# Performance work log

Hardware: AMD Instinct MI355X
Metric: run time of the kernel (lower is better)

The kernel has to match this reference:

```python
import jax, jax.numpy as jnp
import numpy as np

OUT_FEATURES = 8192
PACKED_IN = 4096          # in_features = 2 * PACKED_IN = 8192
GROUP_SIZE = 128
N_GROUPS = (2 * PACKED_IN) // GROUP_SIZE  # 64


def _unpack_int4(packed):
    """Unpack bytes (stored as int32 in [0,256)) into signed int4 pairs [O, 2P].

    Matches torch: high nibble first, then low nibble, both sign-corrected
    (values >= 8 map to value - 16).
    """
    high = packed >> 4
    low = packed & 15
    high = jnp.where(high >= 8, high - 16, high)
    low = jnp.where(low >= 8, low - 16, low)
    return jnp.stack([high, low], axis=-1).reshape(packed.shape[0], -1)


def setup_inputs() -> dict:
    key = jax.random.key(0)
    k1, k2, k3, k4, k5 = jax.random.split(key, 5)
    x = jax.random.normal(k1, (1, 128, 2 * PACKED_IN), dtype=jnp.float32)
    weight_q = jax.random.randint(k2, (OUT_FEATURES, PACKED_IN), 0, 256, dtype=jnp.int32)
    # small positive per-group scales, float zero points (as in the torch module)
    scale = jax.random.uniform(k3, (OUT_FEATURES, N_GROUPS), dtype=jnp.float32) * 0.05 + 1e-3
    zero_point = jax.random.normal(k4, (OUT_FEATURES, N_GROUPS), dtype=jnp.float32)
    bias = jax.random.normal(k5, (OUT_FEATURES,), dtype=jnp.float32)
    return {"x": x, "weight_q": weight_q, "scale": scale, "zero_point": zero_point, "bias": bias}


def reference(x, weight_q, scale, zero_point, bias):
    O = weight_q.shape[0]
    w = _unpack_int4(weight_q).astype(jnp.float32)          # [O, in]
    wg = w.reshape(O, N_GROUPS, GROUP_SIZE)                  # group view
    # (w - zp) * scale, broadcast per group (== repeat_interleave in torch)
    W = ((wg - zero_point[:, :, None]) * scale[:, :, None]).reshape(O, -1)
    return jnp.einsum('bsi,oi->bso', x, W) + bias
```

## Files before the change

### kernel.cpp

```cpp
#include <hip/hip_runtime.h>
#include <hip/hip_bf16.h>
#include <stdint.h>

#define M_DIM 128
#define N_DIM 8192
#define K_DIM 8192
#define KP    4096
#define NGRP  64
#define KSPLIT 8
#define KCHUNK (K_DIM / KSPLIT)
#define BK    64
#define NSTEPS (KCHUNK / BK)

typedef __attribute__((ext_vector_type(8))) short bf16x8;
typedef __attribute__((ext_vector_type(4))) float f32x4;

__device__ __forceinline__ unsigned short f2bf(float f) {
  unsigned int u = __float_as_uint(f);
  return (unsigned short)((u + 0x7fffu + ((u >> 16) & 1u)) >> 16);
}

__global__ void xcast_kernel(const float* __restrict__ x, unsigned short* __restrict__ xb) {
  int idx = (blockIdx.x * blockDim.x + threadIdx.x) * 8;
  const float4* xp = (const float4*)(x + idx);
  float4 a = xp[0], b = xp[1];
  uint4 o;
  o.x = (unsigned)f2bf(a.x) | ((unsigned)f2bf(a.y) << 16);
  o.y = (unsigned)f2bf(a.z) | ((unsigned)f2bf(a.w) << 16);
  o.z = (unsigned)f2bf(b.x) | ((unsigned)f2bf(b.y) << 16);
  o.w = (unsigned)f2bf(b.z) | ((unsigned)f2bf(b.w) << 16);
  *(uint4*)(xb + idx) = o;
}

__global__ __launch_bounds__(512, 4)
void gemm_kernel(const unsigned short* __restrict__ xb,
                 const int* __restrict__ wq,
                 const float* __restrict__ scale,
                 const float* __restrict__ zpt,
                 unsigned short* __restrict__ partial)
{
  __shared__ uint4 xtile[2][1024];
  __shared__ uint4 wtile[2][1024];

  const int tid = threadIdx.x;
  const int l   = tid & 63;
  const int w   = tid >> 6;
  const int wm  = w >> 2;
  const int wn  = w & 3;
  const int l15 = l & 15;
  const int lk  = l >> 4;
  const int n0  = blockIdx.x * 128;
  const int ks  = blockIdx.y;
  const int k0  = ks * KCHUNK;

  const int r0 = n0 + wn * 32 + l15;
  const int r1 = r0 + 16;

  const float* sp0 = scale + r0 * NGRP + ks * 8;
  const float* zp0 = zpt   + r0 * NGRP + ks * 8;
  const float* sp1 = scale + r1 * NGRP + ks * 8;
  const float* zp1 = zpt   + r1 * NGRP + ks * 8;
  float4 s0a = *(const float4*)sp0,     s0b = *(const float4*)(sp0 + 4);
  float4 z0a = *(const float4*)zp0,     z0b = *(const float4*)(zp0 + 4);
  float4 s1a = *(const float4*)sp1,     s1b = *(const float4*)(sp1 + 4);
  float4 z1a = *(const float4*)zp1,     z1b = *(const float4*)(zp1 + 4);

  auto STAGE = [&](int t, int nb) {
    const int kt = k0 + t * BK;
    #pragma unroll
    for (int i = 0; i < 2; ++i) {
      int c = i * 512 + tid;
      int row = c >> 3, q = (c & 7) ^ (row & 7);
      const unsigned short* src = xb + (size_t)row * K_DIM + kt + q * 8;
      uint4* dst = &xtile[nb][i * 512 + w * 64];
      __builtin_amdgcn_global_load_lds(
          (__attribute__((address_space(1))) void*)(void*)src,
          (__attribute__((address_space(3))) void*)(void*)dst, 16, 0, 0);
    }
    #pragma unroll
    for (int i = 0; i < 2; ++i) {
      int c = i * 512 + tid;
      int row = c >> 3, q = (c & 7) ^ (row & 7);
      const int* src = wq + (size_t)(n0 + row) * KP + (k0 >> 1) + t * 32 + q * 4;
      uint4* dst = &wtile[nb][i * 512 + w * 64];
      __builtin_amdgcn_global_load_lds(
          (__attribute__((address_space(1))) void*)(void*)src,
          (__attribute__((address_space(3))) void*)(void*)dst, 16, 0, 0);
    }
  };

  f32x4 acc[4][2];
  #pragma unroll
  for (int mi = 0; mi < 4; ++mi)
    #pragma unroll
    for (int ni = 0; ni < 2; ++ni) {
      f32x4 z = {0.f, 0.f, 0.f, 0.f};
      acc[mi][ni] = z;
    }

  STAGE(0, 0);
  STAGE(1, 1);
  float scs0[8] = {s0a.x, s0a.y, s0a.z, s0a.w, s0b.x, s0b.y, s0b.z, s0b.w};
  float scs1[8] = {s1a.x, s1a.y, s1a.z, s1a.w, s1b.x, s1b.y, s1b.z, s1b.w};
  float nzs0[8] = {-z0a.x * s0a.x, -z0a.y * s0a.y, -z0a.z * s0a.z, -z0a.w * s0a.w,
                   -z0b.x * s0b.x, -z0b.y * s0b.y, -z0b.z * s0b.z, -z0b.w * s0b.w};
  float nzs1[8] = {-z1a.x * s1a.x, -z1a.y * s1a.y, -z1a.z * s1a.z, -z1a.w * s1a.w,
                   -z1b.x * s1b.x, -z1b.y * s1b.y, -z1b.z * s1b.z, -z1b.w * s1b.w};

  const int wrow0 = wn * 32 + l15;
  const int wrow1 = wrow0 + 16;

  #pragma unroll
  for (int t = 0; t < NSTEPS; ++t) {
    asm volatile("s_waitcnt vmcnt(4)" ::: "memory");
    __builtin_amdgcn_s_barrier();

    const int cb = t & 1;
    const float sc[2] = {scs0[t >> 1], scs1[t >> 1]};
    const float nz[2] = {nzs0[t >> 1], nzs1[t >> 1]};

    #pragma unroll
    for (int kk = 0; kk < 2; ++kk) {
      const int q = kk * 4 + lk;
      uint4 av[4];
      #pragma unroll
      for (int mi = 0; mi < 4; ++mi) {
        int r = wm * 64 + mi * 16 + l15;
        av[mi] = xtile[cb][r * 8 + (q ^ (r & 7))];
      }
      uint4 pw[2];
      pw[0] = wtile[cb][wrow0 * 8 + (q ^ (wrow0 & 7))];
      pw[1] = wtile[cb][wrow1 * 8 + (q ^ (wrow1 & 7))];
      uint4 bq[2];
      #pragma unroll
      for (int ni = 0; ni < 2; ++ni) {
        int v4[4] = {(int)pw[ni].x, (int)pw[ni].y, (int)pw[ni].z, (int)pw[ni].w};
        unsigned words[4];
        #pragma unroll
        for (int j = 0; j < 4; ++j) {
          int hi = (v4[j] << 24) >> 28;
          int lo = (v4[j] << 28) >> 28;
          float fh = fmaf((float)hi, sc[ni], nz[ni]);
          float fl = fmaf((float)lo, sc[ni], nz[ni]);
          asm("v_cvt_pk_bf16_f32 %0, %1, %2" : "=v"(words[j]) : "v"(fh), "v"(fl));
        }
        uint4 o; o.x = words[0]; o.y = words[1]; o.z = words[2]; o.w = words[3];
        bq[ni] = o;
      }
      #pragma unroll
      for (int mi = 0; mi < 4; ++mi)
        #pragma unroll
        for (int ni = 0; ni < 2; ++ni)
          acc[mi][ni] = __builtin_amdgcn_mfma_f32_16x16x32_bf16(
              __builtin_bit_cast(bf16x8, av[mi]),
              __builtin_bit_cast(bf16x8, bq[ni]),
              acc[mi][ni], 0, 0, 0);
    }

    __builtin_amdgcn_s_barrier();
    STAGE(t + 2 < NSTEPS ? t + 2 : NSTEPS - 1, t & 1);
  }
  asm volatile("s_waitcnt vmcnt(0)" ::: "memory");

  unsigned short* p = partial + (size_t)ks * (M_DIM * N_DIM);
  #pragma unroll
  for (int mi = 0; mi < 4; ++mi)
    #pragma unroll
    for (int ni = 0; ni < 2; ++ni) {
      int col = n0 + wn * 32 + ni * 16 + l15;
      int rowb = wm * 64 + mi * 16 + lk * 4;
      #pragma unroll
      for (int j = 0; j < 4; ++j)
        p[(size_t)(rowb + j) * N_DIM + col] = f2bf(acc[mi][ni][j]);
    }
}

__global__ void reduce_kernel(const unsigned short* __restrict__ part,
                              const float* __restrict__ bias,
                              float* __restrict__ out) {
  int idx = (blockIdx.x * blockDim.x + threadIdx.x) * 8;
  float s[8];
  #pragma unroll
  for (int j = 0; j < 8; ++j) s[j] = 0.f;
  #pragma unroll
  for (int k = 0; k < KSPLIT; ++k) {
    uint4 v = *(const uint4*)(part + (size_t)k * (M_DIM * N_DIM) + idx);
    unsigned ws[4] = {v.x, v.y, v.z, v.w};
    #pragma unroll
    for (int j = 0; j < 4; ++j) {
      s[2 * j]     += __uint_as_float((ws[j] & 0xffffu) << 16);
      s[2 * j + 1] += __uint_as_float(ws[j] & 0xffff0000u);
    }
  }
  int col = idx & (N_DIM - 1);
  float4 b0 = *(const float4*)(bias + col);
  float4 b1 = *(const float4*)(bias + col + 4);
  float4 o0, o1;
  o0.x = s[0] + b0.x; o0.y = s[1] + b0.y; o0.z = s[2] + b0.z; o0.w = s[3] + b0.w;
  o1.x = s[4] + b1.x; o1.y = s[5] + b1.y; o1.z = s[6] + b1.z; o1.w = s[7] + b1.w;
  *(float4*)(out + idx) = o0;
  *(float4*)(out + idx + 4) = o1;
}

extern "C" void kernel_launch(void* const* d_in, const int* in_sizes, int n_in,
                              void* d_out, int out_size, void* d_ws, size_t ws_size,
                              hipStream_t stream) {
  const float* x     = (const float*)d_in[0];
  const int*   wq    = (const int*)d_in[1];
  const float* scale = (const float*)d_in[2];
  const float* zpt   = (const float*)d_in[3];
  const float* bias  = (const float*)d_in[4];
  float* out = (float*)d_out;

  unsigned short* xb = (unsigned short*)d_ws;
  const size_t xbytes = (size_t)M_DIM * K_DIM * 2;
  unsigned short* partial = (unsigned short*)((char*)d_ws + xbytes);

  xcast_kernel<<<(M_DIM * K_DIM) / (256 * 8), 256, 0, stream>>>(x, xb);
  gemm_kernel<<<dim3(N_DIM / 128, KSPLIT), 512, 0, stream>>>(
      xb, wq, scale, zpt, partial);
  reduce_kernel<<<(M_DIM * N_DIM) / (256 * 8), 256, 0, stream>>>(
      partial, bias, out);
}
```

Before: 46.81 us.

## Widen GEMM N tile to 256 to reuse each activation tile across more columns

Doubles the per-block output-column tile from 128 to 256, so each wave computes a 64x64 sub-tile (4x4 MFMA accumulators) instead of 64x32. Each activation tile loaded into LDS is now reused across twice as many weight rows, halving total activation traffic and the grid size. In exchange, register and LDS use per block rise, the launch bound drops to 2 blocks per CU, and the grid shrinks to 256 blocks, which may underfill the GPU's compute units. The wait count is raised to match the extra weight loads per stage.

```diff
diff --git a/kernel.cpp b/kernel.cpp
--- a/kernel.cpp
+++ b/kernel.cpp
@@ -10,6 +10,7 @@
 #define KSPLIT 8
 #define KCHUNK (K_DIM / KSPLIT)
 #define BK    64
+#define BN    256
 #define NSTEPS (KCHUNK / BK)
 
 typedef __attribute__((ext_vector_type(8))) short bf16x8;
@@ -32,7 +33,7 @@
   *(uint4*)(xb + idx) = o;
 }
 
-__global__ __launch_bounds__(512, 4)
+__global__ __launch_bounds__(512, 2)
 void gemm_kernel(const unsigned short* __restrict__ xb,
                  const int* __restrict__ wq,
                  const float* __restrict__ scale,
@@ -40,7 +41,7 @@
                  unsigned short* __restrict__ partial)
 {
   __shared__ uint4 xtile[2][1024];
-  __shared__ uint4 wtile[2][1024];
+  __shared__ uint4 wtile[2][2048];
 
   const int tid = threadIdx.x;
   const int l   = tid & 63;
@@ -49,21 +50,22 @@
   const int wn  = w & 3;
   const int l15 = l & 15;
   const int lk  = l >> 4;
-  const int n0  = blockIdx.x * 128;
+  const int n0  = blockIdx.x * BN;
   const int ks  = blockIdx.y;
   const int k0  = ks * KCHUNK;
 
-  const int r0 = n0 + wn * 32 + l15;
-  const int r1 = r0 + 16;
-
-  const float* sp0 = scale + r0 * NGRP + ks * 8;
-  const float* zp0 = zpt   + r0 * NGRP + ks * 8;
-  const float* sp1 = scale + r1 * NGRP + ks * 8;
-  const float* zp1 = zpt   + r1 * NGRP + ks * 8;
-  float4 s0a = *(const float4*)sp0,     s0b = *(const float4*)(sp0 + 4);
-  float4 z0a = *(const float4*)zp0,     z0b = *(const float4*)(zp0 + 4);
-  float4 s1a = *(const float4*)sp1,     s1b = *(const float4*)(sp1 + 4);
-  float4 z1a = *(const float4*)zp1,     z1b = *(const float4*)(zp1 + 4);
+  int rr[4];
+  #pragma unroll
+  for (int ni = 0; ni < 4; ++ni) rr[ni] = n0 + wn * 64 + ni * 16 + l15;
+
+  float4 sv[4][2], zv[4][2];
+  #pragma unroll
+  for (int ni = 0; ni < 4; ++ni) {
+    const float* sp = scale + rr[ni] * NGRP + ks * 8;
+    const float* zp = zpt   + rr[ni] * NGRP + ks * 8;
+    sv[ni][0] = *(const float4*)sp;  sv[ni][1] = *(const float4*)(sp + 4);
+    zv[ni][0] = *(const float4*)zp;  zv[ni][1] = *(const float4*)(zp + 4);
+  }
 
   auto STAGE = [&](int t, int nb) {
     const int kt = k0 + t * BK;
@@ -78,7 +80,7 @@
           (__attribute__((address_space(3))) void*)(void*)dst, 16, 0, 0);
     }
     #pragma unroll
-    for (int i = 0; i < 2; ++i) {
+    for (int i = 0; i < 4; ++i) {
       int c = i * 512 + tid;
       int row = c >> 3, q = (c & 7) ^ (row & 7);
       const int* src = wq + (size_t)(n0 + row) * KP + (k0 >> 1) + t * 32 + q * 4;
@@ -89,35 +91,36 @@
     }
   };
 
-  f32x4 acc[4][2];
+  f32x4 acc[4][4];
   #pragma unroll
   for (int mi = 0; mi < 4; ++mi)
     #pragma unroll
-    for (int ni = 0; ni < 2; ++ni) {
+    for (int ni = 0; ni < 4; ++ni) {
       f32x4 z = {0.f, 0.f, 0.f, 0.f};
       acc[mi][ni] = z;
     }
 
   STAGE(0, 0);
   STAGE(1, 1);
-  float scs0[8] = {s0a.x, s0a.y, s0a.z, s0a.w, s0b.x, s0b.y, s0b.z, s0b.w};
-  float scs1[8] = {s1a.x, s1a.y, s1a.z, s1a.w, s1b.x, s1b.y, s1b.z, s1b.w};
-  float nzs0[8] = {-z0a.x * s0a.x, -z0a.y * s0a.y, -z0a.z * s0a.z, -z0a.w * s0a.w,
-                   -z0b.x * s0b.x, -z0b.y * s0b.y, -z0b.z * s0b.z, -z0b.w * s0b.w};
-  float nzs1[8] = {-z1a.x * s1a.x, -z1a.y * s1a.y, -z1a.z * s1a.z, -z1a.w * s1a.w,
-                   -z1b.x * s1b.x, -z1b.y * s1b.y, -z1b.z * s1b.z, -z1b.w * s1b.w};
-
-  const int wrow0 = wn * 32 + l15;
-  const int wrow1 = wrow0 + 16;
+  float scs[4][8], nzs[4][8];
+  #pragma unroll
+  for (int ni = 0; ni < 4; ++ni)
+    #pragma unroll
+    for (int h = 0; h < 2; ++h) {
+      float4 s4 = sv[ni][h], z4 = zv[ni][h];
+      scs[ni][h * 4 + 0] = s4.x;  nzs[ni][h * 4 + 0] = -z4.x * s4.x;
+      scs[ni][h * 4 + 1] = s4.y;  nzs[ni][h * 4 + 1] = -z4.y * s4.y;
+      scs[ni][h * 4 + 2] = s4.z;  nzs[ni][h * 4 + 2] = -z4.z * s4.z;
+      scs[ni][h * 4 + 3] = s4.w;  nzs[ni][h * 4 + 3] = -z4.w * s4.w;
+    }
 
   #pragma unroll
   for (int t = 0; t < NSTEPS; ++t) {
-    asm volatile("s_waitcnt vmcnt(4)" ::: "memory");
+    asm volatile("s_waitcnt vmcnt(6)" ::: "memory");
     __builtin_amdgcn_s_barrier();
 
     const int cb = t & 1;
-    const float sc[2] = {scs0[t >> 1], scs1[t >> 1]};
-    const float nz[2] = {nzs0[t >> 1], nzs1[t >> 1]};
+    const int g  = t >> 1;
 
     #pragma unroll
     for (int kk = 0; kk < 2; ++kk) {
@@ -128,20 +131,23 @@
         int r = wm * 64 + mi * 16 + l15;
         av[mi] = xtile[cb][r * 8 + (q ^ (r & 7))];
       }
-      uint4 pw[2];
-      pw[0] = wtile[cb][wrow0 * 8 + (q ^ (wrow0 & 7))];
-      pw[1] = wtile[cb][wrow1 * 8 + (q ^ (wrow1 & 7))];
-      uint4 bq[2];
-      #pragma unroll
-      for (int ni = 0; ni < 2; ++ni) {
+      uint4 pw[4];
+      #pragma unroll
+      for (int ni = 0; ni < 4; ++ni) {
+        int wrow = wn * 64 + ni * 16 + l15;
+        pw[ni] = wtile[cb][wrow * 8 + (q ^ (wrow & 7))];
+      }
+      uint4 bq[4];
+      #pragma unroll
+      for (int ni = 0; ni < 4; ++ni) {
         int v4[4] = {(int)pw[ni].x, (int)pw[ni].y, (int)pw[ni].z, (int)pw[ni].w};
         unsigned words[4];
         #pragma unroll
         for (int j = 0; j < 4; ++j) {
           int hi = (v4[j] << 24) >> 28;
           int lo = (v4[j] << 28) >> 28;
-          float fh = fmaf((float)hi, sc[ni], nz[ni]);
-          float fl = fmaf((float)lo, sc[ni], nz[ni]);
+          float fh = fmaf((float)hi, scs[ni][g], nzs[ni][g]);
+          float fl = fmaf((float)lo, scs[ni][g], nzs[ni][g]);
           asm("v_cvt_pk_bf16_f32 %0, %1, %2" : "=v"(words[j]) : "v"(fh), "v"(fl));
         }
         uint4 o; o.x = words[0]; o.y = words[1]; o.z = words[2]; o.w = words[3];
@@ -150,7 +156,7 @@
       #pragma unroll
       for (int mi = 0; mi < 4; ++mi)
         #pragma unroll
-        for (int ni = 0; ni < 2; ++ni)
+        for (int ni = 0; ni < 4; ++ni)
           acc[mi][ni] = __builtin_amdgcn_mfma_f32_16x16x32_bf16(
               __builtin_bit_cast(bf16x8, av[mi]),
               __builtin_bit_cast(bf16x8, bq[ni]),
@@ -166,8 +172,8 @@
   #pragma unroll
   for (int mi = 0; mi < 4; ++mi)
     #pragma unroll
-    for (int ni = 0; ni < 2; ++ni) {
-      int col = n0 + wn * 32 + ni * 16 + l15;
+    for (int ni = 0; ni < 4; ++ni) {
+      int col = n0 + wn * 64 + ni * 16 + l15;
       int rowb = wm * 64 + mi * 16 + lk * 4;
       #pragma unroll
       for (int j = 0; j < 4; ++j)
@@ -217,7 +223,7 @@
   unsigned short* partial = (unsigned short*)((char*)d_ws + xbytes);
 
   xcast_kernel<<<(M_DIM * K_DIM) / (256 * 8), 256, 0, stream>>>(x, xb);
-  gemm_kernel<<<dim3(N_DIM / 128, KSPLIT), 512, 0, stream>>>(
+  gemm_kernel<<<dim3(N_DIM / BN, KSPLIT), 512, 0, stream>>>(
       xb, wq, scale, zpt, partial);
   reduce_kernel<<<(M_DIM * N_DIM) / (256 * 8), 256, 0, stream>>>(
       partial, bias, out);
```

Result: slower. 52.02 us (+11.1%).
